# Optimization experiments

Hardware: AMD Instinct MI355X
Metric: run time of the kernel (lower is better)

The kernel has to match this reference:

```python
import jax, jax.numpy as jnp
import numpy as np

N = 50000   # nodes
E = 800000  # edges
F_IN = 512
H = 128     # per-hop hidden width
ORDER = 3   # hops (iterations 1..3)
C = 16      # classes


def spmm(idx, vals, x):
    """Sparse [N,N] @ dense [N,d] via COO edges: out[r] += vals[e] * x[c]."""
    row, col = idx[0], idx[1]
    return jax.ops.segment_sum(vals[:, None] * x[col], row, num_segments=x.shape[0])


def setup_inputs() -> dict:
    key = jax.random.key(0)
    ks = jax.random.split(key, 9)
    x = jax.random.normal(ks[0], (N, F_IN), jnp.float32)
    adj_indices = jax.random.randint(ks[1], (2, E), 0, N)
    adj_values = jax.random.uniform(ks[2], (E,), jnp.float32)
    w1 = jax.random.normal(ks[3], (ORDER, F_IN, H), jnp.float32) * 0.05
    b1 = jax.random.normal(ks[4], (ORDER, 1, H), jnp.float32) * 0.05
    w2 = jax.random.normal(ks[5], (ORDER, ORDER * H, H), jnp.float32) * 0.05
    b2 = jax.random.normal(ks[6], (ORDER, 1, H), jnp.float32) * 0.05
    wf = jax.random.normal(ks[7], (ORDER * H, C), jnp.float32) * 0.05
    bf = jnp.zeros((C,), jnp.float32)
    return dict(x=x, adj_indices=adj_indices, adj_values=adj_values,
                w1=w1, b1=b1, w2=w2, b2=b2, wf=wf, bf=bf)


def reference(x, adj_indices, adj_values, w1, b1, w2, b2, wf, bf):
    # Upper: SparseNGCNLayer_i (iterations = i+1): XW + b -> relu -> (i) spmm hops.
    # Dropout is identity in eval mode.
    feats1 = []
    for i in range(ORDER):
        h = jax.nn.relu(x @ w1[i] + b1[i])  # [N, H]
        for _ in range(i):
            h = spmm(adj_indices, adj_values, h)
        feats1.append(h)
    a1 = jnp.concatenate(feats1, axis=1)  # [N, 3H]

    # Bottom: DenseNGCNLayer_i: AW -> (i) spmm hops -> + bias.
    feats2 = []
    for i in range(ORDER):
        h = a1 @ w2[i]  # [N, H]
        for _ in range(i):
            h = spmm(adj_indices, adj_values, h)
        feats2.append(h + b2[i])
    a2 = jnp.concatenate(feats2, axis=1)  # [N, 3H]

    return jax.nn.log_softmax(a2 @ wf + bf, axis=1)  # [N, C]
```

## Files before the change

kernel.cpp:

```cpp
#include <hip/hip_runtime.h>
#include <hip/hip_bf16.h>
#include <cstdint>
#include <cstddef>

#define N_NODES 50000
#define N_EDGES 800000
#define FIN 512
#define HW_ 128
#define NCLS 16
#define SCAN_NB 196

typedef __attribute__((ext_vector_type(4))) float floatx4;
typedef __attribute__((ext_vector_type(4))) int int4v;
typedef __bf16 bf16x8 __attribute__((ext_vector_type(8)));

__device__ __forceinline__ void glds16(const __bf16* g, __bf16* l) {
  __builtin_amdgcn_global_load_lds(
      (const __attribute__((address_space(1))) void*)g,
      (__attribute__((address_space(3))) void*)l, 16, 0, 0);
}

#define RP_NRANK 782
#define PREP_NT1 48
#define PREP_NU 120
__global__ __launch_bounds__(256) void k_rank_prep(
    const int* __restrict__ idx, int* __restrict__ cnt, int* __restrict__ rank,
    const float* __restrict__ w1, __bf16* __restrict__ w1t,
    const float* __restrict__ w2, const float* __restrict__ wf,
    __bf16* __restrict__ Ut,
    const float* __restrict__ b2, const float* __restrict__ bfv,
    float* __restrict__ cc) {
  int b = blockIdx.x;
  int tid = threadIdx.x;
  if (b < RP_NRANK) {
    int e = b * 1024 + tid;
#pragma unroll
    for (int u = 0; u < 4; u++) {
      int ee = e + u * 256;
      if (ee < N_EDGES) rank[ee] = atomicAdd(&cnt[idx[ee]], 1);
    }
  } else if (b < RP_NRANK + PREP_NT1) {
    int tb = b - RP_NRANK;
    const int K = FIN;
    int tilesK = K >> 6;
    int i = tb / (tilesK * 2);
    int rr = tb - i * tilesK * 2;
    int kt = rr >> 1;
    int nt = rr & 1;
    const float* wS = w1 + (size_t)i * K * 128;
    __bf16* wtS = w1t + (size_t)i * 128 * K;
    int k0 = kt * 64, n0 = nt * 64;
    __shared__ float tile[64][65];
    int tc = tid & 63, tr = tid >> 6;
#pragma unroll
    for (int q = 0; q < 16; q++) {
      int row = tr + q * 4;
      tile[row][tc] = wS[(size_t)(k0 + row) * 128 + n0 + tc];
    }
    __syncthreads();
#pragma unroll
    for (int q = 0; q < 16; q++) {
      int nr = tr + q * 4;
      wtS[(size_t)(n0 + nr) * K + k0 + tc] = (__bf16)tile[tc][nr];
    }
  } else if (b < RP_NRANK + PREP_NT1 + PREP_NU) {
    int t = (b - RP_NRANK - PREP_NT1) * 256 + tid;
    int col = t / 384;
    int q = t - col * 384;
    int p = col >> 4, c = col & 15;
    int j = q >> 7;
    int i = p - j;
    float val = 0.f;
    if (i >= 0 && i <= 2) {
      const float* w2row = w2 + ((size_t)i * 384 + q) * 128;
      const float* wfcol = wf + (size_t)128 * i * NCLS + c;
      for (int m = 0; m < 128; m++) val += w2row[m] * wfcol[m * NCLS];
    }
    Ut[(size_t)col * 384 + q] = (__bf16)val;
  } else {
    int c = tid;
    if (c < NCLS) {
      float s = bfv[c];
      for (int k = 0; k < 384; k++) s += b2[k] * wf[k * NCLS + c];
      cc[c] = s;
    }
  }
}

__global__ __launch_bounds__(256) void k_scan_block(const int* __restrict__ cnt,
                                                    int* __restrict__ bsum) {
  int t = blockIdx.x * 256 + threadIdx.x;
  int v = (t < N_NODES) ? cnt[t] : 0;
#pragma unroll
  for (int o = 32; o >= 1; o >>= 1) v += __shfl_down(v, o);
  __shared__ int ws[4];
  if ((threadIdx.x & 63) == 0) ws[threadIdx.x >> 6] = v;
  __syncthreads();
  if (threadIdx.x == 0) bsum[blockIdx.x] = ws[0] + ws[1] + ws[2] + ws[3];
}

__global__ __launch_bounds__(256) void k_scan_fill(const int* __restrict__ cnt,
                                                   const int* __restrict__ bsum,
                                                   int* __restrict__ rowptr) {
  int tid = threadIdx.x;
  int lane = tid & 63;
  int pv = (tid < blockIdx.x && tid < SCAN_NB) ? bsum[tid] : 0;
#pragma unroll
  for (int o = 32; o >= 1; o >>= 1) pv += __shfl_down(pv, o);
  __shared__ int ps[4];
  if (lane == 0) ps[tid >> 6] = pv;
  int t = blockIdx.x * 256 + tid;
  int c = (t < N_NODES) ? cnt[t] : 0;
  int v = c;
#pragma unroll
  for (int o = 1; o < 64; o <<= 1) {
    int n = __shfl_up(v, o);
    if (lane >= o) v += n;
  }
  __shared__ int wt[4];
  if (lane == 63) wt[tid >> 6] = v;
  __syncthreads();
  int add = ps[0] + ps[1] + ps[2] + ps[3];
  for (int w = 0; w < (tid >> 6); w++) add += wt[w];
  int ex = v - c + add;
  if (t < N_NODES) rowptr[t] = ex;
  if (t == 0) rowptr[N_NODES] = N_EDGES;
}

__global__ __launch_bounds__(256) void k_place(
    const int* __restrict__ idx, const float* __restrict__ vals,
    const int* __restrict__ rank, const int* __restrict__ rowptr,
    int2* __restrict__ epack) {
  int e = blockIdx.x * 256 + threadIdx.x;
  if (e < N_EDGES) {
    int r = idx[e];
    int c = idx[N_EDGES + e];
    int p = rowptr[r] + rank[e];
    epack[p] = make_int2(c, __float_as_int(vals[e]));
  }
}

#define G1_TRIOS 391
#define G1_TPX 49
__global__ __launch_bounds__(256) void gemm1(
    const float* __restrict__ A,
    const __bf16* __restrict__ Bt,
    const float* __restrict__ bias,
    __bf16* __restrict__ hb) {
  const int M = N_NODES, K = FIN;
  __shared__ __align__(16) __bf16 sA[2 * 128 * 32];
  __shared__ __align__(16) __bf16 sB[2 * 128 * 32];
  int tid = threadIdx.x;
  int id = blockIdx.x;
  int xcd = id & 7, slot = id >> 3;
  int trio = xcd * G1_TPX + slot / 3;
  int blk = slot - (slot / 3) * 3;
  if (trio >= G1_TRIOS) return;
  int m0 = trio * 128;
  const __bf16* Bblk = Bt + (size_t)blk * 128 * K;
  int wave = tid >> 6, lane = tid & 63;
  int wm = (wave & 1) * 64, wn = (wave >> 1) * 64;
  floatx4 acc[4][4] = {};

  int rA = lane >> 2;
  int gch = (lane & 3) ^ ((lane >> 3) & 3);
  int r0 = wave * 32 + rA;
  int r1 = r0 + 16;
  int gm0 = m0 + r0; gm0 = (gm0 < M) ? gm0 : (M - 1);
  int gm1 = m0 + r1; gm1 = (gm1 < M) ? gm1 : (M - 1);
  const float* pa0 = A + (size_t)gm0 * K + gch * 8;
  const float* pa1 = A + (size_t)gm1 * K + gch * 8;
  const __bf16* pb0 = Bblk + (size_t)r0 * K + gch * 8;
  const __bf16* pb1 = Bblk + (size_t)r1 * K + gch * 8;
  int lofsA = wave * 1024 + lane * 8;
  int lofsB = wave * 1024;

  int fm = lane & 15, fg = lane >> 4;
  int sloto = (fg ^ ((fm >> 1) & 3)) * 8;

  {
    floatx4 x0a = *(const floatx4*)(pa0);
    floatx4 x0b = *(const floatx4*)(pa0 + 4);
    floatx4 x1a = *(const floatx4*)(pa1);
    floatx4 x1b = *(const floatx4*)(pa1 + 4);
    glds16(pb0, sB + lofsB);
    glds16(pb1, sB + lofsB + 512);
    union { bf16x8 v; int4v i; } u0, u1;
#pragma unroll
    for (int q = 0; q < 4; q++) {
      u0.v[q] = (__bf16)x0a[q]; u0.v[q + 4] = (__bf16)x0b[q];
      u1.v[q] = (__bf16)x1a[q]; u1.v[q + 4] = (__bf16)x1b[q];
    }
    *(int4v*)(sA + lofsA) = u0.i;
    *(int4v*)(sA + lofsA + 512) = u1.i;
  }
  __syncthreads();

  for (int t = 0; t < 15; t++) {
    int cb = (t & 1) * 4096;
    int nb = cb ^ 4096;
    int k1 = t * 32 + 32;
    floatx4 n0a = *(const floatx4*)(pa0 + k1);
    floatx4 n0b = *(const floatx4*)(pa0 + k1 + 4);
    floatx4 n1a = *(const floatx4*)(pa1 + k1);
    floatx4 n1b = *(const floatx4*)(pa1 + k1 + 4);
    glds16(pb0 + k1, sB + nb + lofsB);
    glds16(pb1 + k1, sB + nb + lofsB + 512);

    bf16x8 af[4], bfr[4];
#pragma unroll
    for (int mt = 0; mt < 4; mt++)
      af[mt] = *(const bf16x8*)(sA + cb + (wm + mt * 16 + fm) * 32 + sloto);
#pragma unroll
    for (int nt = 0; nt < 4; nt++)
      bfr[nt] = *(const bf16x8*)(sB + cb + (wn + nt * 16 + fm) * 32 + sloto);
#pragma unroll
    for (int mt = 0; mt < 4; mt++)
#pragma unroll
      for (int nt = 0; nt < 4; nt++)
        acc[mt][nt] = __builtin_amdgcn_mfma_f32_16x16x32_bf16(af[mt], bfr[nt], acc[mt][nt], 0, 0, 0);

    union { bf16x8 v; int4v i; } u0, u1;
#pragma unroll
    for (int q = 0; q < 4; q++) {
      u0.v[q] = (__bf16)n0a[q]; u0.v[q + 4] = (__bf16)n0b[q];
      u1.v[q] = (__bf16)n1a[q]; u1.v[q + 4] = (__bf16)n1b[q];
    }
    *(int4v*)(sA + nb + lofsA) = u0.i;
    *(int4v*)(sA + nb + lofsA + 512) = u1.i;
    __syncthreads();
  }
  {
    int cb = 4096;
    bf16x8 af[4], bfr[4];
#pragma unroll
    for (int mt = 0; mt < 4; mt++)
      af[mt] = *(const bf16x8*)(sA + cb + (wm + mt * 16 + fm) * 32 + sloto);
#pragma unroll
    for (int nt = 0; nt < 4; nt++)
      bfr[nt] = *(const bf16x8*)(sB + cb + (wn + nt * 16 + fm) * 32 + sloto);
#pragma unroll
    for (int mt = 0; mt < 4; mt++)
#pragma unroll
      for (int nt = 0; nt < 4; nt++)
        acc[mt][nt] = __builtin_amdgcn_mfma_f32_16x16x32_bf16(af[mt], bfr[nt], acc[mt][nt], 0, 0, 0);
  }

  int colb = lane & 15, rbase = (lane >> 4) << 2;
#pragma unroll
  for (int mt = 0; mt < 4; mt++)
#pragma unroll
    for (int r = 0; r < 4; r++) {
      int gm = m0 + wm + mt * 16 + rbase + r;
      if (gm >= M) continue;
#pragma unroll
      for (int nt = 0; nt < 4; nt++) {
        int gc = blk * 128 + wn + nt * 16 + colb;
        float vv = acc[mt][nt][r] + bias[gc];
        vv = fmaxf(vv, 0.f);
        hb[(size_t)gm * 384 + gc] = (__bf16)vv;
      }
    }
}

__global__ __launch_bounds__(256) void k_sgemm(
    const __bf16* __restrict__ hb,
    const __bf16* __restrict__ Ut,
    float* __restrict__ S,
    float* __restrict__ R4) {
  const int M = N_NODES;
  int wave = threadIdx.x >> 6, lane = threadIdx.x & 63;
  int fm = lane & 15, fg = lane >> 4;
  int m0 = blockIdx.x * 128 + wave * 32;
  floatx4 acc[2][5] = {};
  int r0 = m0 + fm;      r0 = (r0 < M) ? r0 : (M - 1);
  int r1 = m0 + 16 + fm; r1 = (r1 < M) ? r1 : (M - 1);
  const __bf16* pa0 = hb + (size_t)r0 * 384 + fg * 8;
  const __bf16* pa1 = hb + (size_t)r1 * 384 + fg * 8;
  const __bf16* pb  = Ut + (size_t)fm * 384 + fg * 8;
#pragma unroll 2
  for (int k0 = 0; k0 < 384; k0 += 32) {
    bf16x8 a0 = *(const bf16x8*)(pa0 + k0);
    bf16x8 a1 = *(const bf16x8*)(pa1 + k0);
#pragma unroll
    for (int nt = 0; nt < 5; nt++) {
      bf16x8 bv = *(const bf16x8*)(pb + (size_t)nt * 16 * 384 + k0);
      acc[0][nt] = __builtin_amdgcn_mfma_f32_16x16x32_bf16(bv, a0, acc[0][nt], 0, 0, 0);
      acc[1][nt] = __builtin_amdgcn_mfma_f32_16x16x32_bf16(bv, a1, acc[1][nt], 0, 0, 0);
    }
  }
  int gm0 = m0 + fm;
  if (gm0 < M) {
#pragma unroll
    for (int nt = 0; nt < 4; nt++)
      *(floatx4*)(S + (size_t)gm0 * 64 + nt * 16 + fg * 4) = acc[0][nt];
    *(floatx4*)(R4 + (size_t)gm0 * 16 + fg * 4) = acc[0][4];
  }
  int gm1 = m0 + 16 + fm;
  if (gm1 < M) {
#pragma unroll
    for (int nt = 0; nt < 4; nt++)
      *(floatx4*)(S + (size_t)gm1 * 64 + nt * 16 + fg * 4) = acc[1][nt];
    *(floatx4*)(R4 + (size_t)gm1 * 16 + fg * 4) = acc[1][4];
  }
}

template <bool FINAL>
__global__ __launch_bounds__(256) void k_hop(
    const int* __restrict__ rowptr, const int2* __restrict__ epack,
    const float* __restrict__ Rin,
    const float* __restrict__ S, int sofs,
    float* __restrict__ Rout,
    const float* __restrict__ cc) {
  int tid = threadIdx.x;
  int rg = tid >> 2, l = tid & 3;
  int row = blockIdx.x * 64 + rg;
  if (row >= N_NODES) return;
  int s = rowptr[row], e = rowptr[row + 1];
  floatx4 a = *(const floatx4*)(S + (size_t)row * 64 + sofs + l * 4);
  for (int i = s; i < e; i += 4) {
    int take = e - i; if (take > 4) take = 4;
    int2 ed = (l < take) ? epack[i + l] : make_int2(0, 0);
#pragma unroll
    for (int j = 0; j < 4; j++) {
      int c = __shfl(ed.x, j, 4);
      float v = __int_as_float(__shfl(ed.y, j, 4));
      floatx4 g = *(const floatx4*)(Rin + (size_t)c * 16 + l * 4);
      a += v * g;
    }
  }
  if (!FINAL) {
    *(floatx4*)(Rout + (size_t)row * 16 + l * 4) = a;
  } else {
    floatx4 ccv = *(const floatx4*)(cc + l * 4);
    a += ccv;
    float m = fmaxf(fmaxf(a[0], a[1]), fmaxf(a[2], a[3]));
    m = fmaxf(m, __shfl_xor(m, 1, 4));
    m = fmaxf(m, __shfl_xor(m, 2, 4));
    float sm = expf(a[0] - m) + expf(a[1] - m) + expf(a[2] - m) + expf(a[3] - m);
    sm += __shfl_xor(sm, 1, 4);
    sm += __shfl_xor(sm, 2, 4);
    float ls = logf(sm);
    floatx4 o;
#pragma unroll
    for (int q = 0; q < 4; q++) o[q] = (a[q] - m) - ls;
    *(floatx4*)(Rout + (size_t)row * 16 + l * 4) = o;
  }
}

extern "C" void kernel_launch(void* const* d_in, const int* in_sizes, int n_in,
                              void* d_out, int out_size, void* d_ws, size_t ws_size,
                              hipStream_t stream) {
  const float* x   = (const float*)d_in[0];
  const int*   adj = (const int*)d_in[1];
  const float* av  = (const float*)d_in[2];
  const float* w1  = (const float*)d_in[3];
  const float* b1  = (const float*)d_in[4];
  const float* w2  = (const float*)d_in[5];
  const float* b2  = (const float*)d_in[6];
  const float* wf  = (const float*)d_in[7];
  const float* bf  = (const float*)d_in[8];
  float* out = (float*)d_out;

  char* ws = (char*)d_ws;
  size_t off = 0;
  auto alloc = [&](size_t bytes) -> void* {
    off = (off + 255) & ~(size_t)255;
    void* p = ws + off;
    off += bytes;
    return p;
  };

  float* S    = (float*)alloc((size_t)N_NODES * 64 * 4);
  float* R4   = (float*)alloc((size_t)N_NODES * 16 * 4);
  float* RA   = (float*)alloc((size_t)N_NODES * 16 * 4);
  float* RB   = (float*)alloc((size_t)N_NODES * 16 * 4);
  __bf16* hb  = (__bf16*)alloc((size_t)N_NODES * 384 * 2);
  __bf16* w1t = (__bf16*)alloc((size_t)3 * 128 * FIN * 2);
  __bf16* Ut  = (__bf16*)alloc((size_t)80 * 384 * 2);
  int* rowptr = (int*)alloc((size_t)(N_NODES + 1) * 4);
  int* cnt    = (int*)alloc((size_t)N_NODES * 4);
  int* bsum   = (int*)alloc((size_t)SCAN_NB * 4);
  int* rankv  = (int*)alloc((size_t)N_EDGES * 4);
  int2* epack = (int2*)alloc((size_t)N_EDGES * 8);
  float* cc   = (float*)alloc(64);

  hipMemsetAsync(cnt, 0, (size_t)N_NODES * 4, stream);
  k_rank_prep<<<RP_NRANK + PREP_NT1 + PREP_NU + 1, 256, 0, stream>>>(
      adj, cnt, rankv, w1, w1t, w2, wf, Ut, b2, bf, cc);
  k_scan_block<<<SCAN_NB, 256, 0, stream>>>(cnt, bsum);
  k_scan_fill<<<SCAN_NB, 256, 0, stream>>>(cnt, bsum, rowptr);
  k_place<<<(N_EDGES + 255) / 256, 256, 0, stream>>>(adj, av, rankv, rowptr, epack);

  gemm1<<<8 * G1_TPX * 3, 256, 0, stream>>>(x, w1t, b1, hb);

  k_sgemm<<<(N_NODES + 127) / 128, 256, 0, stream>>>(hb, Ut, S, R4);

  int hop_grid = (N_NODES + 63) / 64;
  k_hop<false><<<hop_grid, 256, 0, stream>>>(rowptr, epack, R4, S, 48, RB, cc);
  k_hop<false><<<hop_grid, 256, 0, stream>>>(rowptr, epack, RB, S, 32, RA, cc);
  k_hop<false><<<hop_grid, 256, 0, stream>>>(rowptr, epack, RA, S, 16, RB, cc);
  k_hop<true><<<hop_grid, 256, 0, stream>>>(rowptr, epack, RB, S, 0, out, cc);
}
```

Measured before the change: 336.3 us.

## Fuse CSR build and hop chain into cooperative kernels with grid sync

Replaces the memset, rank, two scan and place launches with one cooperative kernel that uses grid-wide syncs between phases. The four separate hop launches become one cooperative kernel with grid.sync between hops. k_sgemm also gets an XCD-aware block-to-tile mapping. The aim is to cut launch overhead and inter-kernel gaps. The cost is cooperative-launch limits, since the hop grid of 782 blocks must be co-resident, and the rank phase now runs with only 196 blocks, which is less parallel.

```diff
diff --git a/kernel.cpp b/kernel.cpp
--- a/kernel.cpp
+++ b/kernel.cpp
@@ -1,7 +1,10 @@
 #include <hip/hip_runtime.h>
 #include <hip/hip_bf16.h>
+#include <hip/hip_cooperative_groups.h>
 #include <cstdint>
 #include <cstddef>
+
+namespace cg = cooperative_groups;
 
 #define N_NODES 50000
 #define N_EDGES 800000
@@ -20,11 +23,9 @@
       (__attribute__((address_space(3))) void*)l, 16, 0, 0);
 }
 
-#define RP_NRANK 782
 #define PREP_NT1 48
 #define PREP_NU 120
-__global__ __launch_bounds__(256) void k_rank_prep(
-    const int* __restrict__ idx, int* __restrict__ cnt, int* __restrict__ rank,
+__global__ __launch_bounds__(256) void k_prep(
     const float* __restrict__ w1, __bf16* __restrict__ w1t,
     const float* __restrict__ w2, const float* __restrict__ wf,
     __bf16* __restrict__ Ut,
@@ -32,15 +33,8 @@
     float* __restrict__ cc) {
   int b = blockIdx.x;
   int tid = threadIdx.x;
-  if (b < RP_NRANK) {
-    int e = b * 1024 + tid;
-#pragma unroll
-    for (int u = 0; u < 4; u++) {
-      int ee = e + u * 256;
-      if (ee < N_EDGES) rank[ee] = atomicAdd(&cnt[idx[ee]], 1);
-    }
-  } else if (b < RP_NRANK + PREP_NT1) {
-    int tb = b - RP_NRANK;
+  if (b < PREP_NT1) {
+    int tb = b;
     const int K = FIN;
     int tilesK = K >> 6;
     int i = tb / (tilesK * 2);
@@ -63,8 +57,8 @@
       int nr = tr + q * 4;
       wtS[(size_t)(n0 + nr) * K + k0 + tc] = (__bf16)tile[tc][nr];
     }
-  } else if (b < RP_NRANK + PREP_NT1 + PREP_NU) {
-    int t = (b - RP_NRANK - PREP_NT1) * 256 + tid;
+  } else if (b < PREP_NT1 + PREP_NU) {
+    int t = (b - PREP_NT1) * 256 + tid;
     int col = t / 384;
     int q = t - col * 384;
     int p = col >> 4, c = col & 15;
@@ -87,56 +81,63 @@
   }
 }
 
-__global__ __launch_bounds__(256) void k_scan_block(const int* __restrict__ cnt,
-                                                    int* __restrict__ bsum) {
-  int t = blockIdx.x * 256 + threadIdx.x;
-  int v = (t < N_NODES) ? cnt[t] : 0;
-#pragma unroll
-  for (int o = 32; o >= 1; o >>= 1) v += __shfl_down(v, o);
-  __shared__ int ws[4];
-  if ((threadIdx.x & 63) == 0) ws[threadIdx.x >> 6] = v;
-  __syncthreads();
-  if (threadIdx.x == 0) bsum[blockIdx.x] = ws[0] + ws[1] + ws[2] + ws[3];
-}
-
-__global__ __launch_bounds__(256) void k_scan_fill(const int* __restrict__ cnt,
-                                                   const int* __restrict__ bsum,
-                                                   int* __restrict__ rowptr) {
+__global__ __launch_bounds__(256) void k_csr(
+    const int* __restrict__ idx, const float* __restrict__ vals,
+    int* __restrict__ cnt, int* __restrict__ rank,
+    int* __restrict__ bsum, int* __restrict__ rowptr,
+    int2* __restrict__ epack) {
+  cg::grid_group grid = cg::this_grid();
   int tid = threadIdx.x;
   int lane = tid & 63;
-  int pv = (tid < blockIdx.x && tid < SCAN_NB) ? bsum[tid] : 0;
-#pragma unroll
-  for (int o = 32; o >= 1; o >>= 1) pv += __shfl_down(pv, o);
-  __shared__ int ps[4];
-  if (lane == 0) ps[tid >> 6] = pv;
   int t = blockIdx.x * 256 + tid;
+  const int STRIDE = SCAN_NB * 256;
+
+  if (t < N_NODES) cnt[t] = 0;
+  grid.sync();
+
+  for (int e = t; e < N_EDGES; e += STRIDE)
+    rank[e] = atomicAdd(&cnt[idx[e]], 1);
+  grid.sync();
+
   int c = (t < N_NODES) ? cnt[t] : 0;
-  int v = c;
-#pragma unroll
-  for (int o = 1; o < 64; o <<= 1) {
-    int n = __shfl_up(v, o);
-    if (lane >= o) v += n;
-  }
-  __shared__ int wt[4];
-  if (lane == 63) wt[tid >> 6] = v;
-  __syncthreads();
-  int add = ps[0] + ps[1] + ps[2] + ps[3];
-  for (int w = 0; w < (tid >> 6); w++) add += wt[w];
-  int ex = v - c + add;
-  if (t < N_NODES) rowptr[t] = ex;
-  if (t == 0) rowptr[N_NODES] = N_EDGES;
-}
-
-__global__ __launch_bounds__(256) void k_place(
-    const int* __restrict__ idx, const float* __restrict__ vals,
-    const int* __restrict__ rank, const int* __restrict__ rowptr,
-    int2* __restrict__ epack) {
-  int e = blockIdx.x * 256 + threadIdx.x;
-  if (e < N_EDGES) {
+  {
+    int v = c;
+#pragma unroll
+    for (int o = 32; o >= 1; o >>= 1) v += __shfl_down(v, o);
+    __shared__ int ws[4];
+    if (lane == 0) ws[tid >> 6] = v;
+    __syncthreads();
+    if (tid == 0) bsum[blockIdx.x] = ws[0] + ws[1] + ws[2] + ws[3];
+  }
+  grid.sync();
+
+  {
+    int pv = (tid < (int)blockIdx.x && tid < SCAN_NB) ? bsum[tid] : 0;
+#pragma unroll
+    for (int o = 32; o >= 1; o >>= 1) pv += __shfl_down(pv, o);
+    __shared__ int ps[4];
+    if (lane == 0) ps[tid >> 6] = pv;
+    int v = c;
+#pragma unroll
+    for (int o = 1; o < 64; o <<= 1) {
+      int n = __shfl_up(v, o);
+      if (lane >= o) v += n;
+    }
+    __shared__ int wt[4];
+    if (lane == 63) wt[tid >> 6] = v;
+    __syncthreads();
+    int add = ps[0] + ps[1] + ps[2] + ps[3];
+    for (int w = 0; w < (tid >> 6); w++) add += wt[w];
+    int ex = v - c + add;
+    if (t < N_NODES) rowptr[t] = ex;
+    if (t == 0) rowptr[N_NODES] = N_EDGES;
+  }
+  grid.sync();
+
+  for (int e = t; e < N_EDGES; e += STRIDE) {
     int r = idx[e];
-    int c = idx[N_EDGES + e];
-    int p = rowptr[r] + rank[e];
-    epack[p] = make_int2(c, __float_as_int(vals[e]));
+    int cc2 = idx[N_EDGES + e];
+    epack[rowptr[r] + rank[e]] = make_int2(cc2, __float_as_int(vals[e]));
   }
 }
 
@@ -269,9 +270,13 @@
     float* __restrict__ S,
     float* __restrict__ R4) {
   const int M = N_NODES;
+  int id = blockIdx.x;
+  int xcd = id & 7, slot = id >> 3;
+  int trio = xcd * G1_TPX + slot;
+  if (trio >= G1_TRIOS) return;
   int wave = threadIdx.x >> 6, lane = threadIdx.x & 63;
   int fm = lane & 15, fg = lane >> 4;
-  int m0 = blockIdx.x * 128 + wave * 32;
+  int m0 = trio * 128 + wave * 32;
   floatx4 acc[2][5] = {};
   int r0 = m0 + fm;      r0 = (r0 < M) ? r0 : (M - 1);
   int r1 = m0 + 16 + fm; r1 = (r1 < M) ? r1 : (M - 1);
@@ -306,46 +311,60 @@
 }
 
 template <bool FINAL>
-__global__ __launch_bounds__(256) void k_hop(
+__device__ __forceinline__ void hop_body(
     const int* __restrict__ rowptr, const int2* __restrict__ epack,
-    const float* __restrict__ Rin,
-    const float* __restrict__ S, int sofs,
-    float* __restrict__ Rout,
-    const float* __restrict__ cc) {
+    const float* __restrict__ Rin, const float* __restrict__ S, int sofs,
+    float* __restrict__ Rout, const float* __restrict__ cc) {
   int tid = threadIdx.x;
   int rg = tid >> 2, l = tid & 3;
   int row = blockIdx.x * 64 + rg;
-  if (row >= N_NODES) return;
-  int s = rowptr[row], e = rowptr[row + 1];
-  floatx4 a = *(const floatx4*)(S + (size_t)row * 64 + sofs + l * 4);
-  for (int i = s; i < e; i += 4) {
-    int take = e - i; if (take > 4) take = 4;
-    int2 ed = (l < take) ? epack[i + l] : make_int2(0, 0);
-#pragma unroll
-    for (int j = 0; j < 4; j++) {
-      int c = __shfl(ed.x, j, 4);
-      float v = __int_as_float(__shfl(ed.y, j, 4));
-      floatx4 g = *(const floatx4*)(Rin + (size_t)c * 16 + l * 4);
-      a += v * g;
-    }
-  }
-  if (!FINAL) {
-    *(floatx4*)(Rout + (size_t)row * 16 + l * 4) = a;
-  } else {
-    floatx4 ccv = *(const floatx4*)(cc + l * 4);
-    a += ccv;
-    float m = fmaxf(fmaxf(a[0], a[1]), fmaxf(a[2], a[3]));
-    m = fmaxf(m, __shfl_xor(m, 1, 4));
-    m = fmaxf(m, __shfl_xor(m, 2, 4));
-    float sm = expf(a[0] - m) + expf(a[1] - m) + expf(a[2] - m) + expf(a[3] - m);
-    sm += __shfl_xor(sm, 1, 4);
-    sm += __shfl_xor(sm, 2, 4);
-    float ls = logf(sm);
-    floatx4 o;
-#pragma unroll
-    for (int q = 0; q < 4; q++) o[q] = (a[q] - m) - ls;
-    *(floatx4*)(Rout + (size_t)row * 16 + l * 4) = o;
-  }
+  if (row < N_NODES) {
+    int s = rowptr[row], e = rowptr[row + 1];
+    floatx4 a = *(const floatx4*)(S + (size_t)row * 64 + sofs + l * 4);
+    for (int i = s; i < e; i += 4) {
+      int take = e - i; if (take > 4) take = 4;
+      int2 ed = (l < take) ? epack[i + l] : make_int2(0, 0);
+#pragma unroll
+      for (int j = 0; j < 4; j++) {
+        int c = __shfl(ed.x, j, 4);
+        float v = __int_as_float(__shfl(ed.y, j, 4));
+        floatx4 g = *(const floatx4*)(Rin + (size_t)c * 16 + l * 4);
+        a += v * g;
+      }
+    }
+    if (!FINAL) {
+      *(floatx4*)(Rout + (size_t)row * 16 + l * 4) = a;
+    } else {
+      floatx4 ccv = *(const floatx4*)(cc + l * 4);
+      a += ccv;
+      float m = fmaxf(fmaxf(a[0], a[1]), fmaxf(a[2], a[3]));
+      m = fmaxf(m, __shfl_xor(m, 1, 4));
+      m = fmaxf(m, __shfl_xor(m, 2, 4));
+      float sm = expf(a[0] - m) + expf(a[1] - m) + expf(a[2] - m) + expf(a[3] - m);
+      sm += __shfl_xor(sm, 1, 4);
+      sm += __shfl_xor(sm, 2, 4);
+      float ls = logf(sm);
+      floatx4 o;
+#pragma unroll
+      for (int q = 0; q < 4; q++) o[q] = (a[q] - m) - ls;
+      *(floatx4*)(Rout + (size_t)row * 16 + l * 4) = o;
+    }
+  }
+}
+
+__global__ __launch_bounds__(256) void k_hops(
+    const int* __restrict__ rowptr, const int2* __restrict__ epack,
+    const float* __restrict__ R4, const float* __restrict__ S,
+    float* __restrict__ RA, float* __restrict__ RB,
+    float* __restrict__ out, const float* __restrict__ cc) {
+  cg::grid_group grid = cg::this_grid();
+  hop_body<false>(rowptr, epack, R4, S, 48, RB, cc);
+  grid.sync();
+  hop_body<false>(rowptr, epack, RB, S, 32, RA, cc);
+  grid.sync();
+  hop_body<false>(rowptr, epack, RA, S, 16, RB, cc);
+  grid.sync();
+  hop_body<true>(rowptr, epack, RB, S, 0, out, cc);
 }
 
 extern "C" void kernel_launch(void* const* d_in, const int* in_sizes, int n_in,
@@ -385,20 +404,24 @@
   int2* epack = (int2*)alloc((size_t)N_EDGES * 8);
   float* cc   = (float*)alloc(64);
 
-  hipMemsetAsync(cnt, 0, (size_t)N_NODES * 4, stream);
-  k_rank_prep<<<RP_NRANK + PREP_NT1 + PREP_NU + 1, 256, 0, stream>>>(
-      adj, cnt, rankv, w1, w1t, w2, wf, Ut, b2, bf, cc);
-  k_scan_block<<<SCAN_NB, 256, 0, stream>>>(cnt, bsum);
-  k_scan_fill<<<SCAN_NB, 256, 0, stream>>>(cnt, bsum, rowptr);
-  k_place<<<(N_EDGES + 255) / 256, 256, 0, stream>>>(adj, av, rankv, rowptr, epack);
+  k_prep<<<PREP_NT1 + PREP_NU + 1, 256, 0, stream>>>(
+      w1, w1t, w2, wf, Ut, b2, bf, cc);
+
+  {
+    void* args[] = {(void*)&adj, (void*)&av, (void*)&cnt, (void*)&rankv,
+                    (void*)&bsum, (void*)&rowptr, (void*)&epack};
+    hipLaunchCooperativeKernel((void*)k_csr, dim3(SCAN_NB), dim3(256),
+                               args, 0, stream);
+  }
 
   gemm1<<<8 * G1_TPX * 3, 256, 0, stream>>>(x, w1t, b1, hb);
 
-  k_sgemm<<<(N_NODES + 127) / 128, 256, 0, stream>>>(hb, Ut, S, R4);
-
-  int hop_grid = (N_NODES + 63) / 64;
-  k_hop<false><<<hop_grid, 256, 0, stream>>>(rowptr, epack, R4, S, 48, RB, cc);
-  k_hop<false><<<hop_grid, 256, 0, stream>>>(rowptr, epack, RB, S, 32, RA, cc);
-  k_hop<false><<<hop_grid, 256, 0, stream>>>(rowptr, epack, RA, S, 16, RB, cc);
-  k_hop<true><<<hop_grid, 256, 0, stream>>>(rowptr, epack, RB, S, 0, out, cc);
-}
+  k_sgemm<<<8 * G1_TPX, 256, 0, stream>>>(hb, Ut, S, R4);
+
+  {
+    void* hargs[] = {(void*)&rowptr, (void*)&epack, (void*)&R4, (void*)&S,
+                     (void*)&RA, (void*)&RB, (void*)&out, (void*)&cc};
+    hipLaunchCooperativeKernel((void*)k_hops, dim3((N_NODES + 63) / 64),
+                               dim3(256), hargs, 0, stream);
+  }
+}
```

New measurement: 691.5 us. +105.7%, slower.
